# Performance work log

Hardware: AMD Instinct MI355X
Metric: run time of the kernel (lower is better)

## Reference

```python
import jax, jax.numpy as jnp
import numpy as np

H = 1024
V = 50257


def setup_inputs() -> dict:
    key = jax.random.key(0)
    ks = jax.random.split(key, 10)
    s = 0.02
    return {
        "x": jax.random.randint(ks[0], (1,), 0, V, dtype=jnp.int32),
        "h0": jax.random.normal(ks[1], (1, 1, H), jnp.float32),
        "c0": jax.random.normal(ks[2], (1, 1, H), jnp.float32),
        "emb": jax.random.normal(ks[3], (V, H), jnp.float32) * s,
        "w_ih": jax.random.normal(ks[4], (4 * H, H), jnp.float32) * s,
        "w_hh": jax.random.normal(ks[5], (4 * H, H), jnp.float32) * s,
        "b_ih": jax.random.normal(ks[6], (4 * H,), jnp.float32) * s,
        "b_hh": jax.random.normal(ks[7], (4 * H,), jnp.float32) * s,
        "w_out": jax.random.normal(ks[8], (V, H), jnp.float32) * s,
        "b_out": jax.random.normal(ks[9], (V,), jnp.float32) * s,
    }


def reference(x, h0, c0, emb, w_ih, w_hh, b_ih, b_hh, w_out, b_out):
    # embedding lookup + view(1,1,-1) + relu -> [1, H]
    e = jax.nn.relu(emb[x].reshape(1, H))
    h = h0[0]  # [1, H]
    c = c0[0]  # [1, H]
    # single LSTM cell step; PyTorch gate order: i, f, g, o
    gates = e @ w_ih.T + b_ih + h @ w_hh.T + b_hh  # [1, 4H]
    i, f, g, o = jnp.split(gates, 4, axis=1)
    c_new = jax.nn.sigmoid(f) * c + jax.nn.sigmoid(i) * jnp.tanh(g)
    h_new = jax.nn.sigmoid(o) * jnp.tanh(c_new)
    # output projection + log-softmax over vocab
    logits = h_new @ w_out.T + b_out  # [1, V]
    out = jax.nn.log_softmax(logits, axis=1)
    return out, (h_new[None, :, :], c_new[None, :, :])
```

## Files before the change

kernel.cpp:

```cpp
#include <hip/hip_runtime.h>
#include <math.h>

#define HH 1024
#define VV 50257
#define NGATES 4096
#define NPART 64

__device__ __forceinline__ float wave_reduce_sum(float v) {
#pragma unroll
    for (int off = 32; off > 0; off >>= 1) v += __shfl_down(v, off, 64);
    return v;
}

__device__ __forceinline__ void wave_reduce_lse(float& m, float& s) {
#pragma unroll
    for (int off = 32; off > 0; off >>= 1) {
        float om = __shfl_down(m, off, 64);
        float os = __shfl_down(s, off, 64);
        float M = fmaxf(m, om);
        s = s * expf(m - M) + os * expf(om - M);
        m = M;
    }
}

__device__ __forceinline__ float sigmoidf(float x) { return 1.0f / (1.0f + expf(-x)); }

__global__ __launch_bounds__(256) void k_gates(
    const int* __restrict__ x, const float* __restrict__ emb,
    const float* __restrict__ h0, const float* __restrict__ w_ih,
    const float* __restrict__ w_hh, const float* __restrict__ b_ih,
    const float* __restrict__ b_hh, float* __restrict__ gates) {
    int gid = (blockIdx.x * 256 + threadIdx.x) >> 6;
    int lane = threadIdx.x & 63;
    if (gid >= NGATES) return;
    const float* e  = emb + (size_t)x[0] * HH;
    const float* wi = w_ih + (size_t)gid * HH;
    const float* wh = w_hh + (size_t)gid * HH;
    float acc = 0.0f;
#pragma unroll
    for (int k = 0; k < 4; ++k) {
        int idx = k * 256 + lane * 4;
        float4 wiv = *reinterpret_cast<const float4*>(wi + idx);
        float4 whv = *reinterpret_cast<const float4*>(wh + idx);
        float4 ev  = *reinterpret_cast<const float4*>(e + idx);
        float4 hv  = *reinterpret_cast<const float4*>(h0 + idx);
        ev.x = fmaxf(ev.x, 0.0f); ev.y = fmaxf(ev.y, 0.0f);
        ev.z = fmaxf(ev.z, 0.0f); ev.w = fmaxf(ev.w, 0.0f);
        acc += wiv.x * ev.x + wiv.y * ev.y + wiv.z * ev.z + wiv.w * ev.w;
        acc += whv.x * hv.x + whv.y * hv.y + whv.z * hv.z + whv.w * hv.w;
    }
    acc = wave_reduce_sum(acc);
    if (lane == 0) gates[gid] = acc + b_ih[gid] + b_hh[gid];
}

__global__ __launch_bounds__(256) void k_cell(
    const float* __restrict__ gates, const float* __restrict__ c0,
    float* __restrict__ out) {
    int j = blockIdx.x * 256 + threadIdx.x;
    if (j >= HH) return;
    float ig = sigmoidf(gates[j]);
    float fg = sigmoidf(gates[HH + j]);
    float gg = tanhf(gates[2 * HH + j]);
    float og = sigmoidf(gates[3 * HH + j]);
    float c = fg * c0[j] + ig * gg;
    float h = og * tanhf(c);
    out[VV + j] = h;
    out[VV + HH + j] = c;
}

__global__ __launch_bounds__(256) void k_logits(
    const float* __restrict__ w_out, const float* __restrict__ b_out,
    const float* __restrict__ h, float* __restrict__ logits) {
    int row = blockIdx.x * 4 + (threadIdx.x >> 6);
    int lane = threadIdx.x & 63;
    if (row >= VV) return;
    const float* w = w_out + (size_t)row * HH;
    float acc = 0.0f;
#pragma unroll
    for (int k = 0; k < 4; ++k) {
        int idx = k * 256 + lane * 4;
        float4 wv = *reinterpret_cast<const float4*>(w + idx);
        float4 hv = *reinterpret_cast<const float4*>(h + idx);
        acc += wv.x * hv.x + wv.y * hv.y + wv.z * hv.z + wv.w * hv.w;
    }
    acc = wave_reduce_sum(acc);
    if (lane == 0) logits[row] = acc + b_out[row];
}

__global__ __launch_bounds__(256) void k_partial(
    const float* __restrict__ logits, float* __restrict__ pm,
    float* __restrict__ ps) {
    __shared__ float sm[4], ss[4];
    int tid = threadIdx.x;
    float m = -1e30f, s = 0.0f;
    for (int i = blockIdx.x * 256 + tid; i < VV; i += NPART * 256) {
        float v = logits[i];
        if (v > m) {
            s = s * expf(m - v) + 1.0f;
            m = v;
        } else {
            s += expf(v - m);
        }
    }
    wave_reduce_lse(m, s);
    if ((tid & 63) == 0) { sm[tid >> 6] = m; ss[tid >> 6] = s; }
    __syncthreads();
    if (tid == 0) {
        float M = sm[0], S = ss[0];
#pragma unroll
        for (int w = 1; w < 4; ++w) {
            float om = sm[w], os = ss[w];
            float MM = fmaxf(M, om);
            S = S * expf(M - MM) + os * expf(om - MM);
            M = MM;
        }
        pm[blockIdx.x] = M;
        ps[blockIdx.x] = S;
    }
}

__global__ __launch_bounds__(256) void k_final(
    const float* __restrict__ logits, const float* __restrict__ pm,
    const float* __restrict__ ps, float* __restrict__ out) {
    __shared__ float sZ;
    int tid = threadIdx.x;
    if (tid < 64) {
        float m = pm[tid];
        float s = ps[tid];
        wave_reduce_lse(m, s);
        if (tid == 0) sZ = m + logf(s);
    }
    __syncthreads();
    float Z = sZ;
    for (int i = blockIdx.x * 256 + tid; i < VV; i += gridDim.x * 256)
        out[i] = logits[i] - Z;
}

extern "C" void kernel_launch(void* const* d_in, const int* in_sizes, int n_in,
                              void* d_out, int out_size, void* d_ws, size_t ws_size,
                              hipStream_t stream) {
    const int*   x     = (const int*)d_in[0];
    const float* h0    = (const float*)d_in[1];
    const float* c0    = (const float*)d_in[2];
    const float* emb   = (const float*)d_in[3];
    const float* w_ih  = (const float*)d_in[4];
    const float* w_hh  = (const float*)d_in[5];
    const float* b_ih  = (const float*)d_in[6];
    const float* b_hh  = (const float*)d_in[7];
    const float* w_out = (const float*)d_in[8];
    const float* b_out = (const float*)d_in[9];
    float* out = (float*)d_out;
    float* ws  = (float*)d_ws;

    float* gates  = ws;
    float* logits = ws + NGATES;
    float* pm     = ws + NGATES + 50304;
    float* ps     = pm + NPART;

    k_gates<<<NGATES / 4, 256, 0, stream>>>(x, emb, h0, w_ih, w_hh, b_ih, b_hh, gates);
    k_cell<<<(HH + 255) / 256, 256, 0, stream>>>(gates, c0, out);
    k_logits<<<(VV + 3) / 4, 256, 0, stream>>>(w_out, b_out, out + VV, logits);
    k_partial<<<NPART, 256, 0, stream>>>(logits, pm, ps);
    k_final<<<256, 256, 0, stream>>>(logits, pm, ps, out);
}
```

Measured before the change: 49.25 us.

## Fuse LSTM gates with cell update and logits with partial log-sum-exp

Each block now computes the four gate rows for one hidden unit and applies the cell update itself, so the separate gates buffer and cell kernel are gone. The output projection is now a persistent-style grid of 2048 blocks that loops over rows and keeps a running max and sum per wave, which removes the separate partial-reduction kernel. The final kernel reduces 2048 partials instead of 64. The kernel count drops from five to three, but the logits kernel's loop reduces the number of waves in flight and adds serial exp work on lane 0.

Result: no change. 48.81 us (-0.9%).

```diff
diff --git a/kernel.cpp b/kernel.cpp
--- a/kernel.cpp
+++ b/kernel.cpp
@@ -3,8 +3,7 @@
 
 #define HH 1024
 #define VV 50257
-#define NGATES 4096
-#define NPART 64
+#define NLB 2048
 
 __device__ __forceinline__ float wave_reduce_sum(float v) {
 #pragma unroll
@@ -25,17 +24,20 @@
 
 __device__ __forceinline__ float sigmoidf(float x) { return 1.0f / (1.0f + expf(-x)); }
 
-__global__ __launch_bounds__(256) void k_gates(
+__global__ __launch_bounds__(256) void k_gatecell(
     const int* __restrict__ x, const float* __restrict__ emb,
-    const float* __restrict__ h0, const float* __restrict__ w_ih,
-    const float* __restrict__ w_hh, const float* __restrict__ b_ih,
-    const float* __restrict__ b_hh, float* __restrict__ gates) {
-    int gid = (blockIdx.x * 256 + threadIdx.x) >> 6;
+    const float* __restrict__ h0, const float* __restrict__ c0,
+    const float* __restrict__ w_ih, const float* __restrict__ w_hh,
+    const float* __restrict__ b_ih, const float* __restrict__ b_hh,
+    float* __restrict__ out) {
+    __shared__ float sg[4];
+    int j = blockIdx.x;
+    int w = threadIdx.x >> 6;
     int lane = threadIdx.x & 63;
-    if (gid >= NGATES) return;
+    int row = w * HH + j;
     const float* e  = emb + (size_t)x[0] * HH;
-    const float* wi = w_ih + (size_t)gid * HH;
-    const float* wh = w_hh + (size_t)gid * HH;
+    const float* wi = w_ih + (size_t)row * HH;
+    const float* wh = w_hh + (size_t)row * HH;
     float acc = 0.0f;
 #pragma unroll
     for (int k = 0; k < 4; ++k) {
@@ -50,66 +52,59 @@
         acc += whv.x * hv.x + whv.y * hv.y + whv.z * hv.z + whv.w * hv.w;
     }
     acc = wave_reduce_sum(acc);
-    if (lane == 0) gates[gid] = acc + b_ih[gid] + b_hh[gid];
+    if (lane == 0) sg[w] = acc + b_ih[row] + b_hh[row];
+    __syncthreads();
+    if (threadIdx.x == 0) {
+        float ig = sigmoidf(sg[0]);
+        float fg = sigmoidf(sg[1]);
+        float gg = tanhf(sg[2]);
+        float og = sigmoidf(sg[3]);
+        float c = fg * c0[j] + ig * gg;
+        float h = og * tanhf(c);
+        out[VV + j] = h;
+        out[VV + HH + j] = c;
+    }
 }
 
-__global__ __launch_bounds__(256) void k_cell(
-    const float* __restrict__ gates, const float* __restrict__ c0,
-    float* __restrict__ out) {
-    int j = blockIdx.x * 256 + threadIdx.x;
-    if (j >= HH) return;
-    float ig = sigmoidf(gates[j]);
-    float fg = sigmoidf(gates[HH + j]);
-    float gg = tanhf(gates[2 * HH + j]);
-    float og = sigmoidf(gates[3 * HH + j]);
-    float c = fg * c0[j] + ig * gg;
-    float h = og * tanhf(c);
-    out[VV + j] = h;
-    out[VV + HH + j] = c;
-}
-
-__global__ __launch_bounds__(256) void k_logits(
+__global__ __launch_bounds__(256) void k_logits_lse(
     const float* __restrict__ w_out, const float* __restrict__ b_out,
-    const float* __restrict__ h, float* __restrict__ logits) {
-    int row = blockIdx.x * 4 + (threadIdx.x >> 6);
+    const float* __restrict__ h, float* __restrict__ logits,
+    float* __restrict__ pm, float* __restrict__ ps) {
+    __shared__ float sm[4], ss[4];
+    int w = threadIdx.x >> 6;
     int lane = threadIdx.x & 63;
-    if (row >= VV) return;
-    const float* w = w_out + (size_t)row * HH;
-    float acc = 0.0f;
+    float m = -1e30f, s = 0.0f;
+    for (int c = 0;; ++c) {
+        int row = c * (NLB * 4) + blockIdx.x * 4 + w;
+        if (row >= VV) break;
+        const float* wr = w_out + (size_t)row * HH;
+        float acc = 0.0f;
 #pragma unroll
-    for (int k = 0; k < 4; ++k) {
-        int idx = k * 256 + lane * 4;
-        float4 wv = *reinterpret_cast<const float4*>(w + idx);
-        float4 hv = *reinterpret_cast<const float4*>(h + idx);
-        acc += wv.x * hv.x + wv.y * hv.y + wv.z * hv.z + wv.w * hv.w;
-    }
-    acc = wave_reduce_sum(acc);
-    if (lane == 0) logits[row] = acc + b_out[row];
-}
-
-__global__ __launch_bounds__(256) void k_partial(
-    const float* __restrict__ logits, float* __restrict__ pm,
-    float* __restrict__ ps) {
-    __shared__ float sm[4], ss[4];
-    int tid = threadIdx.x;
-    float m = -1e30f, s = 0.0f;
-    for (int i = blockIdx.x * 256 + tid; i < VV; i += NPART * 256) {
-        float v = logits[i];
-        if (v > m) {
-            s = s * expf(m - v) + 1.0f;
-            m = v;
-        } else {
-            s += expf(v - m);
+        for (int k = 0; k < 4; ++k) {
+            int idx = k * 256 + lane * 4;
+            float4 wv = *reinterpret_cast<const float4*>(wr + idx);
+            float4 hv = *reinterpret_cast<const float4*>(h + idx);
+            acc += wv.x * hv.x + wv.y * hv.y + wv.z * hv.z + wv.w * hv.w;
+        }
+        acc = wave_reduce_sum(acc);
+        if (lane == 0) {
+            float v = acc + b_out[row];
+            logits[row] = v;
+            if (v > m) {
+                s = s * expf(m - v) + 1.0f;
+                m = v;
+            } else {
+                s += expf(v - m);
+            }
         }
     }
-    wave_reduce_lse(m, s);
-    if ((tid & 63) == 0) { sm[tid >> 6] = m; ss[tid >> 6] = s; }
+    if (lane == 0) { sm[w] = m; ss[w] = s; }
     __syncthreads();
-    if (tid == 0) {
+    if (threadIdx.x == 0) {
         float M = sm[0], S = ss[0];
 #pragma unroll
-        for (int w = 1; w < 4; ++w) {
-            float om = sm[w], os = ss[w];
+        for (int q = 1; q < 4; ++q) {
+            float om = sm[q], os = ss[q];
             float MM = fmaxf(M, om);
             S = S * expf(M - MM) + os * expf(om - MM);
             M = MM;
@@ -122,13 +117,30 @@
 __global__ __launch_bounds__(256) void k_final(
     const float* __restrict__ logits, const float* __restrict__ pm,
     const float* __restrict__ ps, float* __restrict__ out) {
+    __shared__ float sm[4], ss[4];
     __shared__ float sZ;
     int tid = threadIdx.x;
-    if (tid < 64) {
-        float m = pm[tid];
-        float s = ps[tid];
-        wave_reduce_lse(m, s);
-        if (tid == 0) sZ = m + logf(s);
+    int lane = tid & 63;
+    float m = -1e30f, s = 0.0f;
+    for (int p = tid; p < NLB; p += 256) {
+        float om = pm[p], os = ps[p];
+        float M = fmaxf(m, om);
+        s = s * expf(m - M) + os * expf(om - M);
+        m = M;
+    }
+    wave_reduce_lse(m, s);
+    if (lane == 0) { sm[tid >> 6] = m; ss[tid >> 6] = s; }
+    __syncthreads();
+    if (tid == 0) {
+        float M = sm[0], S = ss[0];
+#pragma unroll
+        for (int q = 1; q < 4; ++q) {
+            float om = sm[q], os = ss[q];
+            float MM = fmaxf(M, om);
+            S = S * expf(M - MM) + os * expf(om - MM);
+            M = MM;
+        }
+        sZ = M + logf(S);
     }
     __syncthreads();
     float Z = sZ;
@@ -152,14 +164,11 @@
     float* out = (float*)d_out;
     float* ws  = (float*)d_ws;
 
-    float* gates  = ws;
-    float* logits = ws + NGATES;
-    float* pm     = ws + NGATES + 50304;
-    float* ps     = pm + NPART;
+    float* logits = ws;
+    float* pm     = ws + 50304;
+    float* ps     = pm + NLB;
 
-    k_gates<<<NGATES / 4, 256, 0, stream>>>(x, emb, h0, w_ih, w_hh, b_ih, b_hh, gates);
-    k_cell<<<(HH + 255) / 256, 256, 0, stream>>>(gates, c0, out);
-    k_logits<<<(VV + 3) / 4, 256, 0, stream>>>(w_out, b_out, out + VV, logits);
-    k_partial<<<NPART, 256, 0, stream>>>(logits, pm, ps);
+    k_gatecell<<<HH, 256, 0, stream>>>(x, emb, h0, c0, w_ih, w_hh, b_ih, b_hh, out);
+    k_logits_lse<<<NLB, 256, 0, stream>>>(w_out, b_out, out + VV, logits, pm, ps);
     k_final<<<256, 256, 0, stream>>>(logits, pm, ps, out);
 }
```
